# Performance work log

Measured on AMD Instinct MI355X. Metric: run time of the kernel, lower is better.

The kernel has to match this reference:

```python
import jax, jax.numpy as jnp
import numpy as np

NUM_HEADS = 8
GROUPS = 32  # min(32, 512 // 4)
EPS = 1e-5


def group_norm(y, gamma, beta):
    B, C, L = y.shape
    yg = y.reshape(B, GROUPS, -1)  # [B, G, (C//G)*L]
    mu = yg.mean(-1, keepdims=True)
    var = yg.var(-1, keepdims=True)
    yn = ((yg - mu) * jax.lax.rsqrt(var + EPS)).reshape(B, C, L)
    return yn * gamma[:, None] + beta[:, None]


def setup_inputs() -> dict:
    key = jax.random.key(0)
    ks = jax.random.split(key, 5)
    B, C, L = 4, 512, 2048
    return {
        "x": jax.random.normal(ks[0], (B, C, L), dtype=jnp.float32),
        "Wqkv": jax.random.normal(ks[1], (3 * C, C), dtype=jnp.float32) * (C ** -0.5),
        "bqkv": jax.random.normal(ks[2], (3 * C,), dtype=jnp.float32) * 0.01,
        "Wproj": jax.random.normal(ks[3], (C, C), dtype=jnp.float32) * (C ** -0.5),
        "bproj": jax.random.normal(ks[4], (C,), dtype=jnp.float32) * 0.01,
        "gamma": jnp.ones((C,), dtype=jnp.float32),
        "beta": jnp.zeros((C,), dtype=jnp.float32),
    }


def reference(x, Wqkv, bqkv, Wproj, bproj, gamma, beta):
    B, C, L = x.shape
    H = NUM_HEADS
    D = C // H
    # 1x1 Conv1d == channel-mixing matmul
    qkv = jnp.einsum('oc,bcl->bol', Wqkv, x) + bqkv[:, None]  # [B, 3C, L]
    qkv = qkv.reshape(B, 3, H, D, L)
    q, k, v = qkv[:, 0], qkv[:, 1], qkv[:, 2]
    q = jnp.clip(q, -10.0, 10.0)
    k = jnp.clip(k, -10.0, 10.0)
    v = jnp.clip(v, -10.0, 10.0)
    scale = D ** -0.5
    attn = jnp.einsum('bhdi,bhdj->bhij', q, k) * scale  # [B, H, L, L]
    attn = jnp.clip(attn, -10.0, 10.0)
    attn = jax.nn.softmax(attn, axis=-1)
    # NaN fallback: replace whole attn with identity if any NaN (matches torch branch)
    has_nan = jnp.isnan(attn).any()
    attn = jnp.where(has_nan, jnp.eye(L, dtype=x.dtype), attn)
    out = jnp.einsum('bhij,bhdj->bhdi', attn, v)  # [B, H, D, L]
    out = out.reshape(B, C, L)
    out = jnp.einsum('oc,bcl->bol', Wproj, out) + bproj[:, None]
    return group_norm(out + x, gamma, beta)
```

## Files before the change

### kernel.cpp

```cpp
#include <hip/hip_runtime.h>
#include <cstddef>

#define B_ 4
#define C_ 512
#define L_ 2048

typedef __attribute__((ext_vector_type(8))) short  short8;
typedef __attribute__((ext_vector_type(4))) float  f32x4;
typedef __attribute__((ext_vector_type(4))) unsigned short us4;

#define AS1 __attribute__((address_space(1)))
#define AS3 __attribute__((address_space(3)))

__device__ __forceinline__ float clip10(float v){ return fminf(fmaxf(v,-10.0f),10.0f); }

__device__ __forceinline__ unsigned short f2bf(float f){
  union { float f; unsigned u; } v; v.f = f;
  unsigned r = v.u + 0x7fffu + ((v.u >> 16) & 1u);
  return (unsigned short)(r >> 16);
}
__device__ __forceinline__ unsigned pk_tr(float lo, float hi){
  return __builtin_amdgcn_perm(__float_as_uint(hi), __float_as_uint(lo), 0x07060302u);
}
__device__ __forceinline__ float bf2f(unsigned short u){
  return __uint_as_float(((unsigned)u)<<16);
}
__device__ __forceinline__ void gl16(const void* g, void* l){
  __builtin_amdgcn_global_load_lds((const AS1 unsigned*)g, (AS3 unsigned*)l, 16, 0, 0);
}
__device__ __forceinline__ void drain_dma(){
  asm volatile("s_waitcnt vmcnt(0)" ::: "memory");
}
__device__ __forceinline__ short8 mk8(unsigned a, unsigned b, unsigned c, unsigned d){
  union { unsigned u[4]; short8 s; } v;
  v.u[0]=a; v.u[1]=b; v.u[2]=c; v.u[3]=d;
  return v.s;
}

__global__ __launch_bounds__(256) void prep_k(
    const float* __restrict__ x, const float* __restrict__ Wq,
    const float* __restrict__ Wp, unsigned short* __restrict__ xT,
    unsigned short* __restrict__ Wqb, unsigned short* __restrict__ Wpb,
    float* __restrict__ part)
{
  const int blk = blockIdx.x;
  const int t = threadIdx.x;
  if (blk < 4096){
    __shared__ float tile[32][33];
    const int b = blk>>10, rem = blk&1023;
    const int c0 = (rem>>6)*32, l0 = (rem&63)*32;
    const int cr = t>>3, lc = (t&7)*4;
    const float4 v = *(const float4*)(x + ((size_t)b*C_ + c0+cr)*L_ + l0 + lc);
    tile[cr][lc]=v.x; tile[cr][lc+1]=v.y; tile[cr][lc+2]=v.z; tile[cr][lc+3]=v.w;
    __syncthreads();
    const int lr = t>>3, cc = (t&7)*4;
    const us4 o = { f2bf(tile[cc][lr]), f2bf(tile[cc+1][lr]),
                    f2bf(tile[cc+2][lr]), f2bf(tile[cc+3][lr]) };
    *(us4*)(xT + ((size_t)b*L_ + l0+lr)*C_ + c0 + cc) = o;
  } else if (blk < 5120){
    const int i = (blk-4096)*256 + t;
    const int NQ = 1536*512/4;
    const float* src; unsigned short* dst; int j;
    if (i < NQ){ src = Wq; dst = Wqb; j = i; }
    else       { src = Wp; dst = Wpb; j = i - NQ; }
    const float4 v = *(const float4*)(src + (size_t)j*4);
    const us4 o = { f2bf(v.x), f2bf(v.y), f2bf(v.z), f2bf(v.w) };
    *(us4*)(dst + (size_t)j*4) = o;
  } else {
    part[t] = 0.f;
  }
}

template<int MODE>
__global__ __launch_bounds__(256) void mfma_gemm(
    const unsigned short* __restrict__ Wb, const unsigned short* __restrict__ Bin,
    const float* __restrict__ bias, const float* __restrict__ xres,
    unsigned short* __restrict__ qT, unsigned short* __restrict__ kT,
    unsigned short* __restrict__ vN,
    float* __restrict__ part)
{
  __shared__ unsigned short SA[128*64];
  __shared__ unsigned short SB[128*64];
  const int t = threadIdx.x;
  const int b = blockIdx.z;
  const int mb = blockIdx.y, n0 = blockIdx.x*128, m0 = mb*128;
  const int lane = t&63, w = t>>6, wm = w>>1, wn = w&1;
  const int n = lane&15, q4 = lane>>4;
  const bool SWAP = (MODE==1) || (MODE==0 && mb>=8);

  f32x4 acc[4][4];
#pragma unroll
  for (int i=0;i<4;i++)
#pragma unroll
    for (int j=0;j<4;j++) acc[i][j] = (f32x4){0.f,0.f,0.f,0.f};

  const unsigned short* Arow = Wb + (size_t)m0*512;
  const unsigned short* Brow = Bin + ((size_t)b*L_ + n0)*512;

  for (int kt=0; kt<8; kt++){
    const int k0 = kt*64;
    __syncthreads();
#pragma unroll
    for (int i=0;i<4;i++){
      const int ch = t + 256*i;
      const int row = ch>>3, lc = (ch&7) ^ (row&7);
      gl16(Arow + (size_t)row*512 + k0 + lc*8, &SA[ch*8]);
      gl16(Brow + (size_t)row*512 + k0 + lc*8, &SB[ch*8]);
    }
    drain_dma();
    __syncthreads();
#pragma unroll
    for (int kk=0;kk<2;kk++){
      short8 aF[4], bF[4];
      const int pc = ((kk*4+q4) ^ (n&7))*8;
#pragma unroll
      for (int mt=0;mt<4;mt++) aF[mt] = *(const short8*)&SA[(wm*64+mt*16+n)*64 + pc];
#pragma unroll
      for (int nt=0;nt<4;nt++) bF[nt] = *(const short8*)&SB[(wn*64+nt*16+n)*64 + pc];
      if (SWAP){
#pragma unroll
        for (int mt=0;mt<4;mt++)
#pragma unroll
          for (int nt=0;nt<4;nt++)
            acc[mt][nt] = __builtin_amdgcn_mfma_f32_16x16x32_bf16(bF[nt], aF[mt], acc[mt][nt], 0,0,0);
      } else {
#pragma unroll
        for (int mt=0;mt<4;mt++)
#pragma unroll
          for (int nt=0;nt<4;nt++)
            acc[mt][nt] = __builtin_amdgcn_mfma_f32_16x16x32_bf16(aF[mt], bF[nt], acc[mt][nt], 0,0,0);
      }
    }
  }

  const float QS = 0.180336880f;
  if (MODE==0 && SWAP){
#pragma unroll
    for (int mt=0;mt<4;mt++){
      const int o = m0 + wm*64 + mt*16 + n;
      const float bv = bias[o];
#pragma unroll
      for (int nt=0;nt<4;nt++){
        const int p = ((nt>>1)<<2) | ((q4&1)<<3) | ((q4>>1)<<4) | ((nt&1)<<5);
        const int l = n0 + wn*64 + p;
        const float r0=clip10(acc[mt][nt][0]+bv), r1=clip10(acc[mt][nt][1]+bv),
                    r2=clip10(acc[mt][nt][2]+bv), r3=clip10(acc[mt][nt][3]+bv);
        const us4 ov = { f2bf(r0), f2bf(r1), f2bf(r2), f2bf(r3) };
        *(us4*)&vN[((size_t)b*512 + (o-1024))*L_ + l] = ov;
      }
    }
    return;
  }
  if (MODE==1){
#pragma unroll
    for (int mt=0;mt<4;mt++){
      const int o = m0 + wm*64 + mt*16 + n;
      const float bv = bias[o];
      float gs=0.f, gq=0.f;
#pragma unroll
      for (int nt=0;nt<4;nt++){
        const int l = n0 + wn*64 + nt*16 + q4*4;
        const float4 xv = *(const float4*)(xres + ((size_t)b*512 + o)*L_ + l);
        const float y0=acc[mt][nt][0]+bv+xv.x, y1=acc[mt][nt][1]+bv+xv.y,
                    y2=acc[mt][nt][2]+bv+xv.z, y3=acc[mt][nt][3]+bv+xv.w;
        gs += (y0+y1)+(y2+y3);
        gq += (y0*y0+y1*y1)+(y2*y2+y3*y3);
        const us4 ov = { f2bf(y0), f2bf(y1), f2bf(y2), f2bf(y3) };
        *(us4*)&vN[((size_t)b*512 + o)*L_ + l] = ov;
      }
#pragma unroll
      for (int off=1; off<64; off<<=1){
        gs += __shfl_xor(gs, off);
        gq += __shfl_xor(gq, off);
      }
      if (lane==0){
        const int g = mb*8 + wm*4 + mt;
        atomicAdd(&part[(b*32+g)*2+0], gs);
        atomicAdd(&part[(b*32+g)*2+1], gq);
      }
    }
    return;
  }
#pragma unroll
  for (int mt=0;mt<4;mt++){
    const int obase = m0 + wm*64 + mt*16 + q4*4;
    const float b0=bias[obase], b1=bias[obase+1], b2=bias[obase+2], b3=bias[obase+3];
#pragma unroll
    for (int nt=0;nt<4;nt++){
      const int l = n0 + wn*64 + nt*16 + n;
      float r0=clip10(acc[mt][nt][0]+b0), r1=clip10(acc[mt][nt][1]+b1),
            r2=clip10(acc[mt][nt][2]+b2), r3=clip10(acc[mt][nt][3]+b3);
      const int typ = mb>>2;
      const int oin = obase - typ*512;
      if (typ==0){ r0*=QS; r1*=QS; r2*=QS; r3*=QS; }
      unsigned short* dst = (typ==0) ? qT : kT;
      const us4 o = { f2bf(r0), f2bf(r1), f2bf(r2), f2bf(r3) };
      *(us4*)&dst[((size_t)b*L_ + l)*512 + oin] = o;
    }
  }
}

#define OPX 68

__global__ __launch_bounds__(512,4) void attn_v13(
    const unsigned short* __restrict__ qT, const unsigned short* __restrict__ kT,
    const unsigned short* __restrict__ vN,
    unsigned short* __restrict__ attnT)
{
  __shared__ unsigned short smem[16384];
  const int t  = threadIdx.x;
  const int id  = blockIdx.x;
  const int xcd = id & 7, s = id >> 3;
  const int pr  = xcd*4 + (s & 3);
  const int i0  = (s >> 2) * 128;
  const int h   = pr & 7, b = pr >> 3;
  const int lane = t&63, w = t>>6, n = lane&15, q4 = lane>>4;

  const unsigned short* kb0 = kT + (size_t)b*L_*512 + h*64;
  const unsigned short* vb  = vN + ((size_t)b*512 + h*64)*L_;

  short8 qf[2];
#pragma unroll
  for (int kk=0; kk<2; kk++)
    qf[kk] = *(const short8*)(qT + ((size_t)b*L_ + i0 + w*16 + n)*512
                                 + h*64 + kk*32 + q4*8);

  short8 ones;
#pragma unroll
  for (int i=0;i<8;i++) ones[i] = (short)0x3F80;

  f32x4 oacc[4];
  f32x4 oden = (f32x4){0.f,0.f,0.f,0.f};
#pragma unroll
  for (int dt=0;dt<4;dt++) oacc[dt]=(f32x4){0.f,0.f,0.f,0.f};

  const float LIM = 14.4269504089f;

  {
    const int ch = t, row = ch>>3, lc = (ch&7)^(row&7);
    gl16(kb0 + (size_t)row*512 + lc*8, &smem[ch*8]);
    gl16(vb  + (size_t)row*L_ + lc*8,  &smem[4096 + ch*8]);
  }
  drain_dma();
  __syncthreads();

  for (int j0=0; j0<L_; j0+=64){
    const int cur = (j0>>6)&1;
    const unsigned short* sk = &smem[cur*8192];
    const unsigned short* sv = &smem[cur*8192 + 4096];

    if (j0+64 < L_){
      const int nb = cur^1;
      const int ch = t, row = ch>>3, lc = (ch&7)^(row&7);
      gl16(kb0 + (size_t)(j0+64+row)*512 + lc*8, &smem[nb*8192 + ch*8]);
      gl16(vb  + (size_t)row*L_ + j0+64 + lc*8,  &smem[nb*8192+4096 + ch*8]);
    }

    f32x4 sacc[4];
#pragma unroll
    for (int jt=0;jt<4;jt++) sacc[jt]=(f32x4){0.f,0.f,0.f,0.f};
#pragma unroll
    for (int kk=0;kk<2;kk++){
      const int pc = ((kk*4+q4) ^ (n&7))*8;
      short8 aK[4];
#pragma unroll
      for (int jt=0;jt<4;jt++) aK[jt] = *(const short8*)&sk[(jt*16+n)*64 + pc];
#pragma unroll
      for (int jt=0;jt<4;jt++)
        sacc[jt] = __builtin_amdgcn_mfma_f32_16x16x32_bf16(aK[jt], qf[kk], sacc[jt], 0,0,0);
    }

    unsigned pw[4][2];
#pragma unroll
    for (int jt=0;jt<4;jt++){
      const float e0 = __builtin_amdgcn_exp2f(__builtin_amdgcn_fmed3f(sacc[jt][0],-LIM,LIM));
      const float e1 = __builtin_amdgcn_exp2f(__builtin_amdgcn_fmed3f(sacc[jt][1],-LIM,LIM));
      const float e2 = __builtin_amdgcn_exp2f(__builtin_amdgcn_fmed3f(sacc[jt][2],-LIM,LIM));
      const float e3 = __builtin_amdgcn_exp2f(__builtin_amdgcn_fmed3f(sacc[jt][3],-LIM,LIM));
      pw[jt][0] = pk_tr(e0,e1);
      pw[jt][1] = pk_tr(e2,e3);
    }

#pragma unroll
    for (int kk=0;kk<2;kk++){
      const int pcv = ((kk*4+q4) ^ (n&7))*8;
      short8 bV[4];
#pragma unroll
      for (int dt=0;dt<4;dt++) bV[dt] = *(const short8*)&sv[(dt*16+n)*64 + pcv];
      const short8 pA = mk8(pw[kk][0], pw[kk][1], pw[kk+2][0], pw[kk+2][1]);
#pragma unroll
      for (int dt=0;dt<4;dt++)
        oacc[dt] = __builtin_amdgcn_mfma_f32_16x16x32_bf16(pA, bV[dt], oacc[dt], 0,0,0);
      oden = __builtin_amdgcn_mfma_f32_16x16x32_bf16(pA, ones, oden, 0,0,0);
    }
    drain_dma();
    __syncthreads();
  }

  float inv[4];
#pragma unroll
  for (int r=0;r<4;r++) inv[r] = 1.0f/oden[r];

  unsigned short* sb = smem;
#pragma unroll
  for (int dt=0;dt<4;dt++)
#pragma unroll
    for (int r=0;r<4;r++)
      sb[(w*16 + q4*4 + r)*OPX + dt*16 + n] = f2bf(oacc[dt][r]*inv[r]);
#pragma unroll
  for (int it=0; it<4; it++){
    const int chunk = it*64 + lane;
    const int row = chunk>>4, c4 = (chunk&15)*4;
    const us4 ov = *(const us4*)&sb[(w*16 + row)*OPX + c4];
    *(us4*)&attnT[((size_t)b*L_ + i0 + w*16 + row)*512 + h*64 + c4] = ov;
  }
}

__global__ __launch_bounds__(256) void gn_apply(
    const unsigned short* __restrict__ yb, const float* __restrict__ part,
    const float* __restrict__ gamma, const float* __restrict__ beta,
    float* __restrict__ out)
{
  const int blk = blockIdx.x;
  const int b = blk>>7, g = (blk>>2)&31, s = blk&3;
  const float sum = part[(b*32+g)*2+0];
  const float sq  = part[(b*32+g)*2+1];
  const float mu = sum*(1.0f/32768.0f);
  const float rs = rsqrtf(sq*(1.0f/32768.0f) - mu*mu + 1e-5f);
  const size_t base = ((size_t)b*C_ + g*16)*L_ + s*512;
  const int t = threadIdx.x;
#pragma unroll
  for (int i=0;i<4;i++){
    const int chunk = i*256 + t;
    const int row = chunk>>6;
    const int lc  = (chunk&63)*8;
    const int c = g*16 + row;
    const float ga = gamma[c]*rs, be = beta[c] - mu*ga;
    const size_t off = base + (size_t)row*L_ + lc;
    const short8 v = *(const short8*)(yb + off);
    float4 r1, r2;
    r1.x = bf2f((unsigned short)v[0])*ga + be;
    r1.y = bf2f((unsigned short)v[1])*ga + be;
    r1.z = bf2f((unsigned short)v[2])*ga + be;
    r1.w = bf2f((unsigned short)v[3])*ga + be;
    r2.x = bf2f((unsigned short)v[4])*ga + be;
    r2.y = bf2f((unsigned short)v[5])*ga + be;
    r2.z = bf2f((unsigned short)v[6])*ga + be;
    r2.w = bf2f((unsigned short)v[7])*ga + be;
    *(float4*)(out+off)   = r1;
    *(float4*)(out+off+4) = r2;
  }
}

extern "C" void kernel_launch(void* const* d_in, const int* in_sizes, int n_in,
                              void* d_out, int out_size, void* d_ws, size_t ws_size,
                              hipStream_t stream)
{
  (void)in_sizes; (void)n_in; (void)out_size; (void)ws_size;
  const float* x     = (const float*)d_in[0];
  const float* Wqkv  = (const float*)d_in[1];
  const float* bqkv  = (const float*)d_in[2];
  const float* Wproj = (const float*)d_in[3];
  const float* bproj = (const float*)d_in[4];
  const float* gamma = (const float*)d_in[5];
  const float* beta  = (const float*)d_in[6];
  float* out = (float*)d_out;
  char* ws = (char*)d_ws;

  const size_t MB = 1024*1024;
  unsigned short* qT    = (unsigned short*)(ws);
  unsigned short* kT    = (unsigned short*)(ws +  8*MB);
  unsigned short* vN    = (unsigned short*)(ws + 16*MB);
  unsigned short* attnT = (unsigned short*)(ws + 24*MB);
  unsigned short* xT    = (unsigned short*)(ws + 32*MB);
  unsigned short* Wqb   = (unsigned short*)(ws + 42*MB);
  unsigned short* Wpb   = (unsigned short*)(ws + 44*MB);
  unsigned short* yb    = (unsigned short*)(ws + 45*MB);
  float*          part  = (float*)        (ws + 61*MB);

  prep_k      <<<dim3(5121),   256,0,stream>>>(x, Wqkv, Wproj, xT, Wqb, Wpb, part);
  mfma_gemm<0><<<dim3(16,12,4),256,0,stream>>>(Wqb, xT,    bqkv , nullptr, qT,kT,vN, nullptr);
  attn_v13    <<<dim3(512),    512,0,stream>>>(qT, kT, vN, attnT);
  mfma_gemm<1><<<dim3(16, 4,4),256,0,stream>>>(Wpb, attnT, bproj, x, nullptr,nullptr, yb, part);
  gn_apply    <<<dim3(512),    256,0,stream>>>(yb, part, gamma, beta, out);
}
```

Before: 175.5 us.

## Split attention key range across two wave groups with LDS reduction

The attention kernel now launches 1024 threads per block. Two groups of 8 waves each process half of the key/value sequence (1024 keys) with their own double-buffered LDS region, halving the serial loop length per wave. Partial output accumulators and denominators from the second group are written to LDS and summed by the first group before normalization and store. This doubles LDS use per block and adds a reduction step and extra barriers. Occupancy per CU may fall with the larger blocks.

```diff
diff --git a/kernel.cpp b/kernel.cpp
--- a/kernel.cpp
+++ b/kernel.cpp
@@ -201,13 +201,14 @@
 }
 
 #define OPX 68
-
-__global__ __launch_bounds__(512,4) void attn_v13(
+#define PPITCH 21
+
+__global__ __launch_bounds__(1024,8) void attn_v15(
     const unsigned short* __restrict__ qT, const unsigned short* __restrict__ kT,
     const unsigned short* __restrict__ vN,
     unsigned short* __restrict__ attnT)
 {
-  __shared__ unsigned short smem[16384];
+  __shared__ unsigned short smem[32768];
   const int t  = threadIdx.x;
   const int id  = blockIdx.x;
   const int xcd = id & 7, s = id >> 3;
@@ -215,6 +216,9 @@
   const int i0  = (s >> 2) * 128;
   const int h   = pr & 7, b = pr >> 3;
   const int lane = t&63, w = t>>6, n = lane&15, q4 = lane>>4;
+  const int iw = w & 7;
+  const int jg = w >> 3;
+  const int jbase = jg*1024;
 
   const unsigned short* kb0 = kT + (size_t)b*L_*512 + h*64;
   const unsigned short* vb  = vN + ((size_t)b*512 + h*64)*L_;
@@ -222,7 +226,7 @@
   short8 qf[2];
 #pragma unroll
   for (int kk=0; kk<2; kk++)
-    qf[kk] = *(const short8*)(qT + ((size_t)b*L_ + i0 + w*16 + n)*512
+    qf[kk] = *(const short8*)(qT + ((size_t)b*L_ + i0 + iw*16 + n)*512
                                  + h*64 + kk*32 + q4*8);
 
   short8 ones;
@@ -236,49 +240,50 @@
 
   const float LIM = 14.4269504089f;
 
-  {
-    const int ch = t, row = ch>>3, lc = (ch&7)^(row&7);
-    gl16(kb0 + (size_t)row*512 + lc*8, &smem[ch*8]);
-    gl16(vb  + (size_t)row*L_ + lc*8,  &smem[4096 + ch*8]);
-  }
+  const int tg = t & 511;
+  const int srow = tg>>3, slc = (tg&7)^(srow&7);
+  unsigned short* gbase = &smem[jg*16384];
+
+  gl16(kb0 + (size_t)(jbase+srow)*512 + slc*8, &gbase[tg*8]);
+  gl16(vb  + (size_t)srow*L_ + jbase  + slc*8, &gbase[4096 + tg*8]);
   drain_dma();
   __syncthreads();
 
-  for (int j0=0; j0<L_; j0+=64){
-    const int cur = (j0>>6)&1;
-    const unsigned short* sk = &smem[cur*8192];
-    const unsigned short* sv = &smem[cur*8192 + 4096];
-
-    if (j0+64 < L_){
-      const int nb = cur^1;
-      const int ch = t, row = ch>>3, lc = (ch&7)^(row&7);
-      gl16(kb0 + (size_t)(j0+64+row)*512 + lc*8, &smem[nb*8192 + ch*8]);
-      gl16(vb  + (size_t)row*L_ + j0+64 + lc*8,  &smem[nb*8192+4096 + ch*8]);
+  for (int jt=0; jt<16; jt++){
+    const int cur = jt&1;
+    const unsigned short* sk = &gbase[cur*8192];
+    const unsigned short* sv = &gbase[cur*8192 + 4096];
+
+    if (jt < 15){
+      unsigned short* nb = &gbase[(cur^1)*8192];
+      const int jn = jbase + (jt+1)*64;
+      gl16(kb0 + (size_t)(jn+srow)*512 + slc*8, &nb[tg*8]);
+      gl16(vb  + (size_t)srow*L_ + jn  + slc*8, &nb[4096 + tg*8]);
     }
 
     f32x4 sacc[4];
 #pragma unroll
-    for (int jt=0;jt<4;jt++) sacc[jt]=(f32x4){0.f,0.f,0.f,0.f};
+    for (int j4=0;j4<4;j4++) sacc[j4]=(f32x4){0.f,0.f,0.f,0.f};
 #pragma unroll
     for (int kk=0;kk<2;kk++){
       const int pc = ((kk*4+q4) ^ (n&7))*8;
       short8 aK[4];
 #pragma unroll
-      for (int jt=0;jt<4;jt++) aK[jt] = *(const short8*)&sk[(jt*16+n)*64 + pc];
-#pragma unroll
-      for (int jt=0;jt<4;jt++)
-        sacc[jt] = __builtin_amdgcn_mfma_f32_16x16x32_bf16(aK[jt], qf[kk], sacc[jt], 0,0,0);
+      for (int j4=0;j4<4;j4++) aK[j4] = *(const short8*)&sk[(j4*16+n)*64 + pc];
+#pragma unroll
+      for (int j4=0;j4<4;j4++)
+        sacc[j4] = __builtin_amdgcn_mfma_f32_16x16x32_bf16(aK[j4], qf[kk], sacc[j4], 0,0,0);
     }
 
     unsigned pw[4][2];
 #pragma unroll
-    for (int jt=0;jt<4;jt++){
-      const float e0 = __builtin_amdgcn_exp2f(__builtin_amdgcn_fmed3f(sacc[jt][0],-LIM,LIM));
-      const float e1 = __builtin_amdgcn_exp2f(__builtin_amdgcn_fmed3f(sacc[jt][1],-LIM,LIM));
-      const float e2 = __builtin_amdgcn_exp2f(__builtin_amdgcn_fmed3f(sacc[jt][2],-LIM,LIM));
-      const float e3 = __builtin_amdgcn_exp2f(__builtin_amdgcn_fmed3f(sacc[jt][3],-LIM,LIM));
-      pw[jt][0] = pk_tr(e0,e1);
-      pw[jt][1] = pk_tr(e2,e3);
+    for (int j4=0;j4<4;j4++){
+      const float e0 = __builtin_amdgcn_exp2f(__builtin_amdgcn_fmed3f(sacc[j4][0],-LIM,LIM));
+      const float e1 = __builtin_amdgcn_exp2f(__builtin_amdgcn_fmed3f(sacc[j4][1],-LIM,LIM));
+      const float e2 = __builtin_amdgcn_exp2f(__builtin_amdgcn_fmed3f(sacc[j4][2],-LIM,LIM));
+      const float e3 = __builtin_amdgcn_exp2f(__builtin_amdgcn_fmed3f(sacc[j4][3],-LIM,LIM));
+      pw[j4][0] = pk_tr(e0,e1);
+      pw[j4][1] = pk_tr(e2,e3);
     }
 
 #pragma unroll
@@ -297,22 +302,45 @@
     __syncthreads();
   }
 
+  float* pbuf = (float*)smem;
+  if (jg == 1){
+    const int slot = (iw*64 + lane)*PPITCH;
+#pragma unroll
+    for (int dt=0;dt<4;dt++)
+#pragma unroll
+      for (int r=0;r<4;r++) pbuf[slot + dt*4 + r] = oacc[dt][r];
+#pragma unroll
+    for (int r=0;r<4;r++) pbuf[slot + 16 + r] = oden[r];
+  }
+  __syncthreads();
+  if (jg == 1) return;
+
+  {
+    const int slot = (iw*64 + lane)*PPITCH;
+#pragma unroll
+    for (int dt=0;dt<4;dt++)
+#pragma unroll
+      for (int r=0;r<4;r++) oacc[dt][r] += pbuf[slot + dt*4 + r];
+#pragma unroll
+    for (int r=0;r<4;r++) oden[r] += pbuf[slot + 16 + r];
+  }
+
   float inv[4];
 #pragma unroll
   for (int r=0;r<4;r++) inv[r] = 1.0f/oden[r];
 
-  unsigned short* sb = smem;
+  unsigned short* sb = &smem[21504];
 #pragma unroll
   for (int dt=0;dt<4;dt++)
 #pragma unroll
     for (int r=0;r<4;r++)
-      sb[(w*16 + q4*4 + r)*OPX + dt*16 + n] = f2bf(oacc[dt][r]*inv[r]);
+      sb[(iw*16 + q4*4 + r)*OPX + dt*16 + n] = f2bf(oacc[dt][r]*inv[r]);
 #pragma unroll
   for (int it=0; it<4; it++){
     const int chunk = it*64 + lane;
     const int row = chunk>>4, c4 = (chunk&15)*4;
-    const us4 ov = *(const us4*)&sb[(w*16 + row)*OPX + c4];
-    *(us4*)&attnT[((size_t)b*L_ + i0 + w*16 + row)*512 + h*64 + c4] = ov;
+    const us4 ov = *(const us4*)&sb[(iw*16 + row)*OPX + c4];
+    *(us4*)&attnT[((size_t)b*L_ + i0 + iw*16 + row)*512 + h*64 + c4] = ov;
   }
 }
 
@@ -380,7 +408,7 @@
 
   prep_k      <<<dim3(5121),   256,0,stream>>>(x, Wqkv, Wproj, xT, Wqb, Wpb, part);
   mfma_gemm<0><<<dim3(16,12,4),256,0,stream>>>(Wqb, xT,    bqkv , nullptr, qT,kT,vN, nullptr);
-  attn_v13    <<<dim3(512),    512,0,stream>>>(qT, kT, vN, attnT);
+  attn_v15    <<<dim3(512),   1024,0,stream>>>(qT, kT, vN, attnT);
   mfma_gemm<1><<<dim3(16, 4,4),256,0,stream>>>(Wpb, attnT, bproj, x, nullptr,nullptr, yb, part);
   gn_apply    <<<dim3(512),    256,0,stream>>>(yb, part, gamma, beta, out);
 }
```

Result: no change. 174.7 us (-0.5%).
